# Kernel optimization log

Hardware: AMD Instinct MI355X
Metric: run time of the kernel (lower is better)

Reference implementation:

```python
import jax, jax.numpy as jnp
import numpy as np

N, E, H = 50000, 800000, 128
HQ = H // 4  # 32


def _mlp(x, w1, b1, w2, b2):
    return jax.nn.relu(x @ w1 + b1) @ w2 + b2


def setup_inputs() -> dict:
    key = jax.random.key(0)
    ks = jax.random.split(key, 16)

    def lin(k, fan_in, fan_out):
        lim = 1.0 / np.sqrt(fan_in)
        kw, kb = jax.random.split(k)
        w = jax.random.uniform(kw, (fan_in, fan_out), jnp.float32, -lim, lim)
        b = jax.random.uniform(kb, (fan_out,), jnp.float32, -lim, lim)
        return w, b

    x = jax.random.normal(ks[0], (N, H), jnp.float32)
    pos = jax.random.normal(ks[1], (N, 3), jnp.float32)
    edge_index = jax.random.randint(ks[2], (2, E), 0, N, jnp.int64)

    pw1, pb1 = lin(ks[3], 3, HQ)
    pw2, pb2 = lin(ks[4], HQ, HQ)
    mw1, mb1 = lin(ks[5], 2 * H + HQ, H)
    mw2, mb2 = lin(ks[6], H, H)
    uw1, ub1 = lin(ks[7], 2 * H, H)
    uw2, ub2 = lin(ks[8], H, H)

    return dict(x=x, pos=pos, edge_index=edge_index,
                pw1=pw1, pb1=pb1, pw2=pw2, pb2=pb2,
                mw1=mw1, mb1=mb1, mw2=mw2, mb2=mb2,
                uw1=uw1, ub1=ub1, uw2=uw2, ub2=ub2)


def reference(x, pos, edge_index,
              pw1, pb1, pw2, pb2,
              mw1, mb1, mw2, mb2,
              uw1, ub1, uw2, ub2):
    row, col = edge_index[0], edge_index[1]
    # position features from relative positions [E, 3] -> [E, H//4]
    pos_feat = _mlp(pos[row] - pos[col], pw1, pb1, pw2, pb2)
    # per-edge messages [E, 2H + H//4] -> [E, H]
    msg_in = jnp.concatenate([x[row], x[col], pos_feat], axis=-1)
    messages = _mlp(msg_in, mw1, mb1, mw2, mb2)
    # scatter-add messages into destination nodes (index_add on col)
    agg = jax.ops.segment_sum(messages, col, num_segments=x.shape[0])
    # node update [N, 2H] -> [N, H]
    return _mlp(jnp.concatenate([x, agg], axis=-1), uw1, ub1, uw2, ub2)
```

## Files before the change

kernel.cpp:

```cpp
#include <hip/hip_runtime.h>
#include <hip/hip_bf16.h>

#define NN 50000
#define NE 800000
#define HD 128
#define SCAN_CHUNK 1024
#define SCAN_BLOCKS ((NN + SCAN_CHUNK - 1) / SCAN_CHUNK)
#define NB_NODE 1024
#define NB_HIST ((NE / 2 + 255) / 256)
#define NB_PREP 65

typedef __attribute__((ext_vector_type(8))) short s16x8;
typedef __attribute__((ext_vector_type(4))) float f32x4;

static __device__ __forceinline__ unsigned short f2bf(float f) {
    unsigned int u = __float_as_uint(f);
    u = (u + 0x7FFFu + ((u >> 16) & 1u)) >> 16;
    return (unsigned short)u;
}
static __device__ __forceinline__ float bf2f(unsigned short h) {
    return __uint_as_float(((unsigned int)h) << 16);
}
static __device__ __forceinline__ unsigned int f2bf2(float lo, float hi) {
    __hip_bfloat162 h = __float22bfloat162_rn(make_float2(lo, hi));
    return *reinterpret_cast<unsigned int*>(&h);
}

#define WFENCE() do { asm volatile("s_waitcnt lgkmcnt(0)" ::: "memory"); \
                      __builtin_amdgcn_sched_barrier(0); } while (0)

__global__ __launch_bounds__(256, 3) void setup_kernel(
    const float* __restrict__ x, const float* __restrict__ mw1,
    const float* __restrict__ mb1,
    const float* __restrict__ pw2, const float* __restrict__ pb2,
    const float* __restrict__ mw2, const float* __restrict__ mb2,
    const float* __restrict__ uw1, const int* __restrict__ ei,
    unsigned short* __restrict__ xa, unsigned short* __restrict__ xb,
    float* __restrict__ aggH, int* __restrict__ cnt,
    float* __restrict__ Wpc, float* __restrict__ W3, float* __restrict__ b3)
{
    __shared__ __align__(16) unsigned short sB[128 * 136];
    __shared__ __align__(16) unsigned short sSt[4][16 * 132];
    __shared__ int sIdx64;

    int bid = blockIdx.x;
    int tid = threadIdx.x;

    if (bid >= NB_NODE) {
        int rb = bid - NB_NODE;
        if (rb < NB_HIST) {
            if (tid == 0) {
                int z = 1;
                for (int k = 0; k < 16; ++k) if (ei[2 * k + 1] != 0) z = 0;
                sIdx64 = z;
            }
            __syncthreads();
            int g = rb * 256 + tid;
            if (g >= NE / 2) return;
            int e0 = g * 2;
            int c0, c1;
            if (sIdx64) { int4 q = *(const int4*)&ei[2 * NE + 2 * e0]; c0 = q.x; c1 = q.z; }
            else        { int2 q = *(const int2*)&ei[NE + e0];         c0 = q.x; c1 = q.y; }
            atomicAdd(&cnt[c0], 1);
            atomicAdd(&cnt[c1], 1);
            return;
        }
        rb -= NB_HIST;
        if (rb == 64) {
            for (int idx = tid; idx < 32 * 128; idx += 256) {
                int j = idx >> 7, k = idx & 127;
                float s = 0.f;
                #pragma unroll 8
                for (int i = 0; i < 32; ++i) s += pw2[j * 32 + i] * mw1[(256 + i) * 128 + k];
                Wpc[idx] = s;
            }
            return;
        }
        int idx = rb * 256 + tid;
        {
            int k = idx >> 7, j = idx & 127;
            float s = 0.f;
            #pragma unroll 4
            for (int c = 0; c < 128; ++c)
                s += mw2[k * 128 + c] * uw1[(128 + c) * 128 + j];
            W3[idx] = s;
        }
        if (rb == 0 && tid < 128) {
            int j = tid;
            float s = 0.f;
            #pragma unroll 4
            for (int c = 0; c < 128; ++c)
                s += mb2[c] * uw1[(128 + c) * 128 + j];
            b3[j] = s;
        }
        return;
    }

    {
        f32x4 z = {0.f, 0.f, 0.f, 0.f};
        const int total4 = NN * HD / 4;
        for (int i = bid * 256 + tid; i < total4; i += NB_NODE * 256)
            ((f32x4*)aggH)[i] = z;
    }
    int half = bid & 1;
    for (int idx = tid; idx < 128 * 128; idx += 256) {
        int c = idx & 127, k = idx >> 7;
        sB[c * 136 + k] = f2bf(mw1[(half * 128 + k) * 128 + c]);
    }
    __syncthreads();

    int lane = tid & 63, wv = tid >> 6;
    int r16 = lane & 15, g4 = lane >> 4;
    unsigned short* st = sSt[wv];
    unsigned short* dst = half ? xb : xa;

    float bcr[8];
    #pragma unroll
    for (int tc = 0; tc < 8; ++tc) bcr[tc] = 0.f;
    if (half) {
        #pragma unroll
        for (int tc = 0; tc < 8; ++tc) bcr[tc] = mb1[tc * 16 + r16];
        for (int i = 0; i < 32; ++i) {
            float pv = pb2[i];
            #pragma unroll
            for (int tc = 0; tc < 8; ++tc)
                bcr[tc] = fmaf(pv, mw1[(256 + i) * 128 + tc * 16 + r16], bcr[tc]);
        }
    }

    const int NT = NN / 16;
    const int nb = NB_NODE >> 1;
    const int nbid = bid >> 1;

    for (int t = nbid * 4 + wv; t < NT; t += nb * 4) {
        int r0 = t * 16;
        int row = r0 + r16;
        s16x8 a[4];
        #pragma unroll
        for (int ks = 0; ks < 4; ++ks) {
            const float* p = &x[(size_t)row * HD + ks * 32 + g4 * 8];
            float4 v0 = *(const float4*)p;
            float4 v1 = *(const float4*)(p + 4);
            union { s16x8 v; unsigned int u[4]; } av;
            av.u[0] = f2bf2(v0.x, v0.y); av.u[1] = f2bf2(v0.z, v0.w);
            av.u[2] = f2bf2(v1.x, v1.y); av.u[3] = f2bf2(v1.z, v1.w);
            a[ks] = av.v;
        }
        float hold[4];
        #pragma unroll
        for (int tc = 0; tc < 8; ++tc) {
            int col = tc * 16 + r16;
            float bv = bcr[tc];
            f32x4 acc = {bv, bv, bv, bv};
            #pragma unroll
            for (int ks = 0; ks < 4; ++ks) {
                s16x8 b = *(const s16x8*)&sB[col * 136 + ks * 32 + g4 * 8];
                acc = __builtin_amdgcn_mfma_f32_16x16x32_bf16(a[ks], b, acc, 0, 0, 0);
            }
            if ((tc & 1) == 0) {
                #pragma unroll
                for (int j = 0; j < 4; ++j) hold[j] = acc[j];
            } else {
                #pragma unroll
                for (int j = 0; j < 4; ++j)
                    *(unsigned int*)&st[(g4 * 4 + j) * 132 + r16 * 8 + (tc - 1)] =
                        f2bf2(hold[j], acc[j]);
            }
        }
        WFENCE();
        #pragma unroll
        for (int i = 0; i < 4; ++i) {
            int idx = i * 512 + lane * 8;
            int rr = idx >> 7, cc = idx & 127;
            *(s16x8*)&dst[(size_t)(r0 + rr) * HD + cc] = *(const s16x8*)&st[rr * 132 + cc];
        }
        WFENCE();
    }
}

__global__ void scan1_kernel(const int* __restrict__ cnt, int* __restrict__ cursor,
                             int* __restrict__ bsum)
{
    __shared__ int tot[256];
    int b = blockIdx.x, t = threadIdx.x;
    int i0 = b * SCAN_CHUNK + t * 4;
    int v[4];
    #pragma unroll
    for (int k = 0; k < 4; ++k) v[k] = (i0 + k < NN) ? cnt[i0 + k] : 0;
    tot[t] = v[0] + v[1] + v[2] + v[3];
    __syncthreads();
    if (t == 0) {
        int run = 0;
        for (int i = 0; i < 256; ++i) { int x = tot[i]; tot[i] = run; run += x; }
        bsum[b] = run;
    }
    __syncthreads();
    int p = tot[t];
    #pragma unroll
    for (int k = 0; k < 4; ++k) {
        if (i0 + k < NN) cursor[i0 + k] = p;
        p += v[k];
    }
}

__global__ void scan3_kernel(int* __restrict__ cursor, const int* __restrict__ bsum)
{
    __shared__ int sCarry;
    int b = blockIdx.x, t = threadIdx.x;
    if (t == 0) {
        int run = 0;
        for (int i = 0; i < b; ++i) run += bsum[i];
        sCarry = run;
    }
    __syncthreads();
    int carry = sCarry;
    int i0 = b * SCAN_CHUNK + t * 4;
    #pragma unroll
    for (int k = 0; k < 4; ++k)
        if (i0 + k < NN) cursor[i0 + k] += carry;
}

__global__ void scatter_kernel(const int* __restrict__ ei,
                               int* __restrict__ cursor, int2* __restrict__ sRC)
{
    __shared__ int sIdx64;
    if (threadIdx.x == 0) {
        int z = 1;
        for (int k = 0; k < 16; ++k) if (ei[2 * k + 1] != 0) z = 0;
        sIdx64 = z;
    }
    __syncthreads();
    int g = blockIdx.x * 256 + threadIdx.x;
    if (g >= NE / 2) return;
    int e0 = g * 2;
    int r0, r1, c0, c1;
    if (sIdx64) {
        int4 qr = *(const int4*)&ei[2 * e0];           r0 = qr.x; r1 = qr.z;
        int4 qc = *(const int4*)&ei[2 * NE + 2 * e0];  c0 = qc.x; c1 = qc.z;
    } else {
        int2 qr = *(const int2*)&ei[e0];       r0 = qr.x; r1 = qr.y;
        int2 qc = *(const int2*)&ei[NE + e0];  c0 = qc.x; c1 = qc.y;
    }
    int p0 = atomicAdd(&cursor[c0], 1);
    sRC[p0] = make_int2(r0, c0);
    int p1 = atomicAdd(&cursor[c1], 1);
    sRC[p1] = make_int2(r1, c1);
}

__global__ __launch_bounds__(256, 3) void edge_kernel(
    const float* __restrict__ pos, const int2* __restrict__ sRC,
    const float* __restrict__ pw1, const float* __restrict__ pb1,
    const unsigned short* __restrict__ xa, const unsigned short* __restrict__ xb,
    const float* __restrict__ Wpc,
    float* __restrict__ aggH)
{
    __shared__ __align__(16) unsigned short sT[4][16 * 136];
    __shared__ int sECs[4][16];

    int tid = threadIdx.x;
    int lane = tid & 63, wv = tid >> 6;
    int r16 = lane & 15, g4 = lane >> 4;
    unsigned short* stg = sT[wv];
    int* secw = sECs[wv];

    s16x8 wr[8];
    #pragma unroll
    for (int tc = 0; tc < 8; ++tc) {
        s16x8 w;
        #pragma unroll
        for (int i = 0; i < 8; ++i)
            w[i] = (short)f2bf(Wpc[(g4 * 8 + i) * 128 + tc * 16 + r16]);
        wr[tc] = w;
    }
    float pw10[8], pw11[8], pw12[8], pb1r[8];
    #pragma unroll
    for (int i = 0; i < 8; ++i) {
        int k = g4 * 8 + i;
        pw10[i] = pw1[k]; pw11[i] = pw1[32 + k]; pw12[i] = pw1[64 + k];
        pb1r[i] = pb1[k];
    }

    const int NW = gridDim.x * 4;
    const int NT = NE / 16;
    int gw = blockIdx.x * 4 + wv;
    if (gw >= NT) return;

    int2 rc = sRC[gw * 16 + r16];
    int2 rcN = rc;
    if (gw + NW < NT) rcN = sRC[(gw + NW) * 16 + r16];
    float dp0 = pos[rc.x * 3 + 0] - pos[rc.y * 3 + 0];
    float dp1 = pos[rc.x * 3 + 1] - pos[rc.y * 3 + 1];
    float dp2 = pos[rc.x * 3 + 2] - pos[rc.y * 3 + 2];
    s16x8 ga[4], gb[4];
    #pragma unroll
    for (int j = 0; j < 4; ++j) {
        int gx = __shfl(rc.x, g4 * 4 + j, 64);
        int gy = __shfl(rc.y, g4 * 4 + j, 64);
        ga[j] = *(const s16x8*)&xa[(size_t)gx * HD + r16 * 8];
        gb[j] = *(const s16x8*)&xb[(size_t)gy * HD + r16 * 8];
    }

    for (int t = gw; t < NT; t += NW) {
        bool hn  = (t + NW) < NT;
        bool hn2 = (t + 2 * NW) < NT;

        if (lane < 16) secw[lane] = rc.y;
        union { s16x8 v; unsigned int u[4]; } apf;
        #pragma unroll
        for (int i2 = 0; i2 < 4; ++i2) {
            int i = 2 * i2;
            float v0 = fmaf(dp0, pw10[i], fmaf(dp1, pw11[i], fmaf(dp2, pw12[i], pb1r[i])));
            float v1 = fmaf(dp0, pw10[i+1], fmaf(dp1, pw11[i+1], fmaf(dp2, pw12[i+1], pb1r[i+1])));
            apf.u[i2] = f2bf2(fmaxf(v0, 0.f), fmaxf(v1, 0.f));
        }

        float hold[4];
        #pragma unroll
        for (int tc = 0; tc < 8; ++tc) {
            f32x4 acc;
            #pragma unroll
            for (int j = 0; j < 4; ++j)
                acc[j] = bf2f((unsigned short)ga[j][tc]) + bf2f((unsigned short)gb[j][tc]);
            acc = __builtin_amdgcn_mfma_f32_16x16x32_bf16(apf.v, wr[tc], acc, 0, 0, 0);
            if ((tc & 1) == 0) {
                #pragma unroll
                for (int j = 0; j < 4; ++j) hold[j] = fmaxf(acc[j], 0.f);
            } else {
                #pragma unroll
                for (int j = 0; j < 4; ++j)
                    *(unsigned int*)&stg[(g4 * 4 + j) * 136 + r16 * 8 + (tc - 1)] =
                        f2bf2(hold[j], fmaxf(acc[j], 0.f));
            }
        }
        WFENCE();

        if (hn) {
            #pragma unroll
            for (int j = 0; j < 4; ++j) {
                int gx = __shfl(rcN.x, g4 * 4 + j, 64);
                int gy = __shfl(rcN.y, g4 * 4 + j, 64);
                ga[j] = *(const s16x8*)&xa[(size_t)gx * HD + r16 * 8];
                gb[j] = *(const s16x8*)&xb[(size_t)gy * HD + r16 * 8];
            }
        }

        int2 rcN2 = rcN;
        if (hn2) rcN2 = sRC[(t + 2 * NW) * 16 + r16];
        float dp0N = 0.f, dp1N = 0.f, dp2N = 0.f;
        if (hn) {
            dp0N = pos[rcN.x * 3 + 0] - pos[rcN.y * 3 + 0];
            dp1N = pos[rcN.x * 3 + 1] - pos[rcN.y * 3 + 1];
            dp2N = pos[rcN.x * 3 + 2] - pos[rcN.y * 3 + 2];
        }

        {
            int p0 = (lane & 15) * 8 + (lane >> 4);
            int p1 = p0 + 4;
            int cur = secw[0];
            float run0 = bf2f(stg[p0]);
            float run1 = bf2f(stg[p1]);
            #pragma unroll
            for (int e = 1; e < 16; ++e) {
                int c = secw[e];
                float v0 = bf2f(stg[e * 136 + p0]);
                float v1 = bf2f(stg[e * 136 + p1]);
                if (c != cur) {
                    unsafeAtomicAdd(&aggH[(size_t)cur * HD + lane], run0);
                    unsafeAtomicAdd(&aggH[(size_t)cur * HD + lane + 64], run1);
                    cur = c; run0 = v0; run1 = v1;
                } else { run0 += v0; run1 += v1; }
            }
            unsafeAtomicAdd(&aggH[(size_t)cur * HD + lane], run0);
            unsafeAtomicAdd(&aggH[(size_t)cur * HD + lane + 64], run1);
        }
        WFENCE();

        rc = rcN; rcN = rcN2; dp0 = dp0N; dp1 = dp1N; dp2 = dp2N;
    }
}

__global__ __launch_bounds__(768, 1) void upd_kernel(
    const float* __restrict__ x, const float* __restrict__ aggH,
    const int* __restrict__ cnt,
    const float* __restrict__ uw1, const float* __restrict__ ub1,
    const float* __restrict__ W3, const float* __restrict__ b3,
    const float* __restrict__ uw2, const float* __restrict__ ub2,
    float* __restrict__ out)
{
    __shared__ __align__(16) unsigned short sB1a[128 * 136];
    __shared__ __align__(16) unsigned short sW3l[128 * 136];
    __shared__ __align__(16) unsigned short sB2[128 * 136];
    __shared__ __align__(16) unsigned short sSt[12][16 * 136];

    int tid = threadIdx.x;
    for (int idx = tid; idx < 128 * 128; idx += 768) {
        int c = idx & 127, k = idx >> 7;
        sB1a[c * 136 + k] = f2bf(uw1[k * 128 + c]);
        sW3l[c * 136 + k] = f2bf(W3[k * 128 + c]);
        sB2[c * 136 + k]  = f2bf(uw2[k * 128 + c]);
    }
    __syncthreads();

    int lane = tid & 63, wv = tid >> 6;
    int r16 = lane & 15, g4 = lane >> 4;
    unsigned short* st = sSt[wv];
    float ub1r[8], ub2r[8], b3r[8];
    #pragma unroll
    for (int tc = 0; tc < 8; ++tc) {
        ub1r[tc] = ub1[tc * 16 + r16];
        ub2r[tc] = ub2[tc * 16 + r16];
        b3r[tc]  = b3[tc * 16 + r16];
    }

    const int NT = NN / 16;
    for (int t = blockIdx.x * 12 + wv; t < NT; t += gridDim.x * 12) {
        int r0 = t * 16;
        int row = r0 + r16;
        s16x8 a[8];
        #pragma unroll
        for (int ks = 0; ks < 8; ++ks) {
            const float* p = (ks < 4) ? &x[(size_t)row * HD + ks * 32 + g4 * 8]
                                      : &aggH[(size_t)row * HD + (ks - 4) * 32 + g4 * 8];
            float4 v0 = *(const float4*)p;
            float4 v1 = *(const float4*)(p + 4);
            union { s16x8 v; unsigned int u[4]; } av;
            av.u[0] = f2bf2(v0.x, v0.y); av.u[1] = f2bf2(v0.z, v0.w);
            av.u[2] = f2bf2(v1.x, v1.y); av.u[3] = f2bf2(v1.z, v1.w);
            a[ks] = av.v;
        }
        float cn[4];
        #pragma unroll
        for (int j = 0; j < 4; ++j) cn[j] = (float)cnt[r0 + g4 * 4 + j];

        #pragma unroll
        for (int tc = 0; tc < 8; ++tc) {
            int col = tc * 16 + r16;
            f32x4 acc;
            #pragma unroll
            for (int j = 0; j < 4; ++j) acc[j] = ub1r[tc] + cn[j] * b3r[tc];
            #pragma unroll
            for (int ks = 0; ks < 4; ++ks) {
                s16x8 b = *(const s16x8*)&sB1a[col * 136 + ks * 32 + g4 * 8];
                acc = __builtin_amdgcn_mfma_f32_16x16x32_bf16(a[ks], b, acc, 0, 0, 0);
            }
            #pragma unroll
            for (int ks = 4; ks < 8; ++ks) {
                s16x8 b = *(const s16x8*)&sW3l[col * 136 + (ks - 4) * 32 + g4 * 8];
                acc = __builtin_amdgcn_mfma_f32_16x16x32_bf16(a[ks], b, acc, 0, 0, 0);
            }
            #pragma unroll
            for (int j = 0; j < 4; ++j)
                st[(g4 * 4 + j) * 136 + col] = f2bf(fmaxf(acc[j], 0.f));
        }
        WFENCE();
        s16x8 a2[4];
        #pragma unroll
        for (int ks = 0; ks < 4; ++ks)
            a2[ks] = *(const s16x8*)&st[r16 * 136 + ks * 32 + g4 * 8];
        WFENCE();
        #pragma unroll
        for (int tc = 0; tc < 8; ++tc) {
            int col = tc * 16 + r16;
            float bv = ub2r[tc];
            f32x4 acc = {bv, bv, bv, bv};
            #pragma unroll
            for (int ks = 0; ks < 4; ++ks) {
                s16x8 b = *(const s16x8*)&sB2[col * 136 + ks * 32 + g4 * 8];
                acc = __builtin_amdgcn_mfma_f32_16x16x32_bf16(a2[ks], b, acc, 0, 0, 0);
            }
            #pragma unroll
            for (int j = 0; j < 4; ++j)
                out[(size_t)(r0 + g4 * 4 + j) * HD + col] = acc[j];
        }
    }
}

extern "C" void kernel_launch(void* const* d_in, const int* in_sizes, int n_in,
                              void* d_out, int out_size, void* d_ws, size_t ws_size,
                              hipStream_t stream)
{
    const float* x   = (const float*)d_in[0];
    const float* pos = (const float*)d_in[1];
    const int*   ei  = (const int*)d_in[2];
    const float* pw1 = (const float*)d_in[3];
    const float* pb1 = (const float*)d_in[4];
    const float* pw2 = (const float*)d_in[5];
    const float* pb2 = (const float*)d_in[6];
    const float* mw1 = (const float*)d_in[7];
    const float* mb1 = (const float*)d_in[8];
    const float* mw2 = (const float*)d_in[9];
    const float* mb2 = (const float*)d_in[10];
    const float* uw1 = (const float*)d_in[11];
    const float* ub1 = (const float*)d_in[12];
    const float* uw2 = (const float*)d_in[13];
    const float* ub2 = (const float*)d_in[14];
    float* out = (float*)d_out;

    char* ws = (char*)d_ws;
    float*          aggH   = (float*)(ws);
    unsigned short* xa     = (unsigned short*)(ws + 25600000);
    unsigned short* xb     = (unsigned short*)(ws + 38400000);
    float*          Wpc    = (float*)(ws + 51200000);
    int*            cnt    = (int*)(ws + 51216896);
    int*            cursor = (int*)(ws + 51417600);
    int*            bsum   = (int*)(ws + 51618304);
    int2*           sRC    = (int2*)(ws + 51618560);
    float*          W3     = (float*)(ws + 58018560);
    float*          b3     = (float*)(ws + 58084096);

    hipMemsetAsync(cnt, 0, NN * sizeof(int), stream);
    setup_kernel<<<NB_NODE + NB_HIST + NB_PREP, 256, 0, stream>>>(
        x, mw1, mb1, pw2, pb2, mw2, mb2, uw1, ei,
        xa, xb, aggH, cnt, Wpc, W3, b3);
    scan1_kernel<<<SCAN_BLOCKS, 256, 0, stream>>>(cnt, cursor, bsum);
    scan3_kernel<<<SCAN_BLOCKS, 256, 0, stream>>>(cursor, bsum);
    scatter_kernel<<<(NE / 2 + 255) / 256, 256, 0, stream>>>(ei, cursor, sRC);
    edge_kernel<<<768, 256, 0, stream>>>(pos, sRC, pw1, pb1, xa, xb, Wpc, aggH);
    upd_kernel<<<256, 768, 0, stream>>>(x, aggH, cnt, uw1, ub1, W3, b3, uw2, ub2, out);
}
```

Baseline: 232.2 us.

## Fold histogram into node blocks and move weight precompute into scatter kernel

The degree histogram no longer runs in separate blocks of the setup kernel. Each node block now counts a contiguous slice of edges before its MFMA projection loop. The small weight-product precomputes (Wpc, W3, b3) move out of setup and into the scatter kernel as extra blocks. This rebalances work across kernels so setup runs fewer, heavier blocks and the precompute overlaps with the scatter. In exchange, the node blocks take on atomic-heavy histogram work, which may lengthen their critical path.

After: 215.9 us. -7.0%, faster.

```diff
diff --git a/kernel.cpp b/kernel.cpp
--- a/kernel.cpp
+++ b/kernel.cpp
@@ -7,8 +7,8 @@
 #define SCAN_CHUNK 1024
 #define SCAN_BLOCKS ((NN + SCAN_CHUNK - 1) / SCAN_CHUNK)
 #define NB_NODE 1024
-#define NB_HIST ((NE / 2 + 255) / 256)
-#define NB_PREP 65
+#define EPB ((NE + NB_NODE - 1) / NB_NODE)
+#define NB_SCAT ((NE / 2 + 255) / 256)
 
 typedef __attribute__((ext_vector_type(8))) short s16x8;
 typedef __attribute__((ext_vector_type(4))) float f32x4;
@@ -29,15 +29,12 @@
 #define WFENCE() do { asm volatile("s_waitcnt lgkmcnt(0)" ::: "memory"); \
                       __builtin_amdgcn_sched_barrier(0); } while (0)
 
-__global__ __launch_bounds__(256, 3) void setup_kernel(
+__global__ __launch_bounds__(256, 3) void node_kernel(
     const float* __restrict__ x, const float* __restrict__ mw1,
-    const float* __restrict__ mb1,
-    const float* __restrict__ pw2, const float* __restrict__ pb2,
-    const float* __restrict__ mw2, const float* __restrict__ mb2,
-    const float* __restrict__ uw1, const int* __restrict__ ei,
+    const float* __restrict__ mb1, const float* __restrict__ pb2,
+    const int* __restrict__ ei,
     unsigned short* __restrict__ xa, unsigned short* __restrict__ xb,
-    float* __restrict__ aggH, int* __restrict__ cnt,
-    float* __restrict__ Wpc, float* __restrict__ W3, float* __restrict__ b3)
+    float* __restrict__ aggH, int* __restrict__ cnt)
 {
     __shared__ __align__(16) unsigned short sB[128 * 136];
     __shared__ __align__(16) unsigned short sSt[4][16 * 132];
@@ -46,26 +43,159 @@
     int bid = blockIdx.x;
     int tid = threadIdx.x;
 
-    if (bid >= NB_NODE) {
-        int rb = bid - NB_NODE;
-        if (rb < NB_HIST) {
-            if (tid == 0) {
-                int z = 1;
-                for (int k = 0; k < 16; ++k) if (ei[2 * k + 1] != 0) z = 0;
-                sIdx64 = z;
-            }
-            __syncthreads();
-            int g = rb * 256 + tid;
-            if (g >= NE / 2) return;
-            int e0 = g * 2;
-            int c0, c1;
-            if (sIdx64) { int4 q = *(const int4*)&ei[2 * NE + 2 * e0]; c0 = q.x; c1 = q.z; }
-            else        { int2 q = *(const int2*)&ei[NE + e0];         c0 = q.x; c1 = q.y; }
-            atomicAdd(&cnt[c0], 1);
-            atomicAdd(&cnt[c1], 1);
-            return;
-        }
-        rb -= NB_HIST;
+    {
+        f32x4 z = {0.f, 0.f, 0.f, 0.f};
+        const int total4 = NN * HD / 4;
+        for (int i = bid * 256 + tid; i < total4; i += NB_NODE * 256)
+            ((f32x4*)aggH)[i] = z;
+    }
+    if (tid == 0) {
+        int z = 1;
+        for (int k = 0; k < 16; ++k) if (ei[2 * k + 1] != 0) z = 0;
+        sIdx64 = z;
+    }
+    int half = bid & 1;
+    for (int idx = tid; idx < 128 * 128; idx += 256) {
+        int c = idx & 127, k = idx >> 7;
+        sB[c * 136 + k] = f2bf(mw1[(half * 128 + k) * 128 + c]);
+    }
+    __syncthreads();
+
+    {
+        int he0 = bid * EPB;
+        int he1 = he0 + EPB; if (he1 > NE) he1 = NE;
+        if (sIdx64) {
+            for (int e = he0 + tid; e < he1; e += 256)
+                atomicAdd(&cnt[ei[2 * NE + 2 * e]], 1);
+        } else {
+            for (int e = he0 + tid; e < he1; e += 256)
+                atomicAdd(&cnt[ei[NE + e]], 1);
+        }
+    }
+
+    int lane = tid & 63, wv = tid >> 6;
+    int r16 = lane & 15, g4 = lane >> 4;
+    unsigned short* st = sSt[wv];
+    unsigned short* dst = half ? xb : xa;
+
+    float bcr[8];
+    #pragma unroll
+    for (int tc = 0; tc < 8; ++tc) bcr[tc] = 0.f;
+    if (half) {
+        #pragma unroll
+        for (int tc = 0; tc < 8; ++tc) bcr[tc] = mb1[tc * 16 + r16];
+        for (int i = 0; i < 32; ++i) {
+            float pv = pb2[i];
+            #pragma unroll
+            for (int tc = 0; tc < 8; ++tc)
+                bcr[tc] = fmaf(pv, mw1[(256 + i) * 128 + tc * 16 + r16], bcr[tc]);
+        }
+    }
+
+    const int NT = NN / 16;
+    const int nb = NB_NODE >> 1;
+    const int nbid = bid >> 1;
+
+    for (int t = nbid * 4 + wv; t < NT; t += nb * 4) {
+        int r0 = t * 16;
+        int row = r0 + r16;
+        s16x8 a[4];
+        #pragma unroll
+        for (int ks = 0; ks < 4; ++ks) {
+            const float* p = &x[(size_t)row * HD + ks * 32 + g4 * 8];
+            float4 v0 = *(const float4*)p;
+            float4 v1 = *(const float4*)(p + 4);
+            union { s16x8 v; unsigned int u[4]; } av;
+            av.u[0] = f2bf2(v0.x, v0.y); av.u[1] = f2bf2(v0.z, v0.w);
+            av.u[2] = f2bf2(v1.x, v1.y); av.u[3] = f2bf2(v1.z, v1.w);
+            a[ks] = av.v;
+        }
+        float hold[4];
+        #pragma unroll
+        for (int tc = 0; tc < 8; ++tc) {
+            int col = tc * 16 + r16;
+            float bv = bcr[tc];
+            f32x4 acc = {bv, bv, bv, bv};
+            #pragma unroll
+            for (int ks = 0; ks < 4; ++ks) {
+                s16x8 b = *(const s16x8*)&sB[col * 136 + ks * 32 + g4 * 8];
+                acc = __builtin_amdgcn_mfma_f32_16x16x32_bf16(a[ks], b, acc, 0, 0, 0);
+            }
+            if ((tc & 1) == 0) {
+                #pragma unroll
+                for (int j = 0; j < 4; ++j) hold[j] = acc[j];
+            } else {
+                #pragma unroll
+                for (int j = 0; j < 4; ++j)
+                    *(unsigned int*)&st[(g4 * 4 + j) * 132 + r16 * 8 + (tc - 1)] =
+                        f2bf2(hold[j], acc[j]);
+            }
+        }
+        WFENCE();
+        #pragma unroll
+        for (int i = 0; i < 4; ++i) {
+            int idx = i * 512 + lane * 8;
+            int rr = idx >> 7, cc = idx & 127;
+            *(s16x8*)&dst[(size_t)(r0 + rr) * HD + cc] = *(const s16x8*)&st[rr * 132 + cc];
+        }
+        WFENCE();
+    }
+}
+
+__global__ void scan1_kernel(const int* __restrict__ cnt, int* __restrict__ cursor,
+                             int* __restrict__ bsum)
+{
+    __shared__ int tot[256];
+    int b = blockIdx.x, t = threadIdx.x;
+    int i0 = b * SCAN_CHUNK + t * 4;
+    int v[4];
+    #pragma unroll
+    for (int k = 0; k < 4; ++k) v[k] = (i0 + k < NN) ? cnt[i0 + k] : 0;
+    tot[t] = v[0] + v[1] + v[2] + v[3];
+    __syncthreads();
+    if (t == 0) {
+        int run = 0;
+        for (int i = 0; i < 256; ++i) { int x = tot[i]; tot[i] = run; run += x; }
+        bsum[b] = run;
+    }
+    __syncthreads();
+    int p = tot[t];
+    #pragma unroll
+    for (int k = 0; k < 4; ++k) {
+        if (i0 + k < NN) cursor[i0 + k] = p;
+        p += v[k];
+    }
+}
+
+__global__ void scan3_kernel(int* __restrict__ cursor, const int* __restrict__ bsum)
+{
+    __shared__ int sCarry;
+    int b = blockIdx.x, t = threadIdx.x;
+    if (t == 0) {
+        int run = 0;
+        for (int i = 0; i < b; ++i) run += bsum[i];
+        sCarry = run;
+    }
+    __syncthreads();
+    int carry = sCarry;
+    int i0 = b * SCAN_CHUNK + t * 4;
+    #pragma unroll
+    for (int k = 0; k < 4; ++k)
+        if (i0 + k < NN) cursor[i0 + k] += carry;
+}
+
+__global__ void scatterprep_kernel(
+    const int* __restrict__ ei, int* __restrict__ cursor, int2* __restrict__ sRC,
+    const float* __restrict__ pw2, const float* __restrict__ mw1,
+    const float* __restrict__ mw2, const float* __restrict__ mb2,
+    const float* __restrict__ uw1,
+    float* __restrict__ Wpc, float* __restrict__ W3, float* __restrict__ b3)
+{
+    __shared__ int sIdx64;
+    int bid = blockIdx.x, tid = threadIdx.x;
+
+    if (bid >= NB_SCAT) {
+        int rb = bid - NB_SCAT;
         if (rb == 64) {
             for (int idx = tid; idx < 32 * 128; idx += 256) {
                 int j = idx >> 7, k = idx & 127;
@@ -96,141 +226,13 @@
         return;
     }
 
-    {
-        f32x4 z = {0.f, 0.f, 0.f, 0.f};
-        const int total4 = NN * HD / 4;
-        for (int i = bid * 256 + tid; i < total4; i += NB_NODE * 256)
-            ((f32x4*)aggH)[i] = z;
-    }
-    int half = bid & 1;
-    for (int idx = tid; idx < 128 * 128; idx += 256) {
-        int c = idx & 127, k = idx >> 7;
-        sB[c * 136 + k] = f2bf(mw1[(half * 128 + k) * 128 + c]);
-    }
-    __syncthreads();
-
-    int lane = tid & 63, wv = tid >> 6;
-    int r16 = lane & 15, g4 = lane >> 4;
-    unsigned short* st = sSt[wv];
-    unsigned short* dst = half ? xb : xa;
-
-    float bcr[8];
-    #pragma unroll
-    for (int tc = 0; tc < 8; ++tc) bcr[tc] = 0.f;
-    if (half) {
-        #pragma unroll
-        for (int tc = 0; tc < 8; ++tc) bcr[tc] = mb1[tc * 16 + r16];
-        for (int i = 0; i < 32; ++i) {
-            float pv = pb2[i];
-            #pragma unroll
-            for (int tc = 0; tc < 8; ++tc)
-                bcr[tc] = fmaf(pv, mw1[(256 + i) * 128 + tc * 16 + r16], bcr[tc]);
-        }
-    }
-
-    const int NT = NN / 16;
-    const int nb = NB_NODE >> 1;
-    const int nbid = bid >> 1;
-
-    for (int t = nbid * 4 + wv; t < NT; t += nb * 4) {
-        int r0 = t * 16;
-        int row = r0 + r16;
-        s16x8 a[4];
-        #pragma unroll
-        for (int ks = 0; ks < 4; ++ks) {
-            const float* p = &x[(size_t)row * HD + ks * 32 + g4 * 8];
-            float4 v0 = *(const float4*)p;
-            float4 v1 = *(const float4*)(p + 4);
-            union { s16x8 v; unsigned int u[4]; } av;
-            av.u[0] = f2bf2(v0.x, v0.y); av.u[1] = f2bf2(v0.z, v0.w);
-            av.u[2] = f2bf2(v1.x, v1.y); av.u[3] = f2bf2(v1.z, v1.w);
-            a[ks] = av.v;
-        }
-        float hold[4];
-        #pragma unroll
-        for (int tc = 0; tc < 8; ++tc) {
-            int col = tc * 16 + r16;
-            float bv = bcr[tc];
-            f32x4 acc = {bv, bv, bv, bv};
-            #pragma unroll
-            for (int ks = 0; ks < 4; ++ks) {
-                s16x8 b = *(const s16x8*)&sB[col * 136 + ks * 32 + g4 * 8];
-                acc = __builtin_amdgcn_mfma_f32_16x16x32_bf16(a[ks], b, acc, 0, 0, 0);
-            }
-            if ((tc & 1) == 0) {
-                #pragma unroll
-                for (int j = 0; j < 4; ++j) hold[j] = acc[j];
-            } else {
-                #pragma unroll
-                for (int j = 0; j < 4; ++j)
-                    *(unsigned int*)&st[(g4 * 4 + j) * 132 + r16 * 8 + (tc - 1)] =
-                        f2bf2(hold[j], acc[j]);
-            }
-        }
-        WFENCE();
-        #pragma unroll
-        for (int i = 0; i < 4; ++i) {
-            int idx = i * 512 + lane * 8;
-            int rr = idx >> 7, cc = idx & 127;
-            *(s16x8*)&dst[(size_t)(r0 + rr) * HD + cc] = *(const s16x8*)&st[rr * 132 + cc];
-        }
-        WFENCE();
-    }
-}
-
-__global__ void scan1_kernel(const int* __restrict__ cnt, int* __restrict__ cursor,
-                             int* __restrict__ bsum)
-{
-    __shared__ int tot[256];
-    int b = blockIdx.x, t = threadIdx.x;
-    int i0 = b * SCAN_CHUNK + t * 4;
-    int v[4];
-    #pragma unroll
-    for (int k = 0; k < 4; ++k) v[k] = (i0 + k < NN) ? cnt[i0 + k] : 0;
-    tot[t] = v[0] + v[1] + v[2] + v[3];
-    __syncthreads();
-    if (t == 0) {
-        int run = 0;
-        for (int i = 0; i < 256; ++i) { int x = tot[i]; tot[i] = run; run += x; }
-        bsum[b] = run;
-    }
-    __syncthreads();
-    int p = tot[t];
-    #pragma unroll
-    for (int k = 0; k < 4; ++k) {
-        if (i0 + k < NN) cursor[i0 + k] = p;
-        p += v[k];
-    }
-}
-
-__global__ void scan3_kernel(int* __restrict__ cursor, const int* __restrict__ bsum)
-{
-    __shared__ int sCarry;
-    int b = blockIdx.x, t = threadIdx.x;
-    if (t == 0) {
-        int run = 0;
-        for (int i = 0; i < b; ++i) run += bsum[i];
-        sCarry = run;
-    }
-    __syncthreads();
-    int carry = sCarry;
-    int i0 = b * SCAN_CHUNK + t * 4;
-    #pragma unroll
-    for (int k = 0; k < 4; ++k)
-        if (i0 + k < NN) cursor[i0 + k] += carry;
-}
-
-__global__ void scatter_kernel(const int* __restrict__ ei,
-                               int* __restrict__ cursor, int2* __restrict__ sRC)
-{
-    __shared__ int sIdx64;
-    if (threadIdx.x == 0) {
+    if (tid == 0) {
         int z = 1;
         for (int k = 0; k < 16; ++k) if (ei[2 * k + 1] != 0) z = 0;
         sIdx64 = z;
     }
     __syncthreads();
-    int g = blockIdx.x * 256 + threadIdx.x;
+    int g = bid * 256 + tid;
     if (g >= NE / 2) return;
     int e0 = g * 2;
     int r0, r1, c0, c1;
@@ -509,12 +511,11 @@
     float*          b3     = (float*)(ws + 58084096);
 
     hipMemsetAsync(cnt, 0, NN * sizeof(int), stream);
-    setup_kernel<<<NB_NODE + NB_HIST + NB_PREP, 256, 0, stream>>>(
-        x, mw1, mb1, pw2, pb2, mw2, mb2, uw1, ei,
-        xa, xb, aggH, cnt, Wpc, W3, b3);
+    node_kernel<<<NB_NODE, 256, 0, stream>>>(x, mw1, mb1, pb2, ei, xa, xb, aggH, cnt);
     scan1_kernel<<<SCAN_BLOCKS, 256, 0, stream>>>(cnt, cursor, bsum);
     scan3_kernel<<<SCAN_BLOCKS, 256, 0, stream>>>(cursor, bsum);
-    scatter_kernel<<<(NE / 2 + 255) / 256, 256, 0, stream>>>(ei, cursor, sRC);
+    scatterprep_kernel<<<NB_SCAT + 65, 256, 0, stream>>>(
+        ei, cursor, sRC, pw2, mw1, mw2, mb2, uw1, Wpc, W3, b3);
     edge_kernel<<<768, 256, 0, stream>>>(pos, sRC, pw1, pb1, xa, xb, Wpc, aggH);
     upd_kernel<<<256, 768, 0, stream>>>(x, aggH, cnt, uw1, ub1, W3, b3, uw2, ub2, out);
 }
```
